# Kernel tuning notes

Hardware: AMD Instinct MI355X
Metric: run time of the kernel (lower is better)

The kernel has to match this reference:

```python
import jax, jax.numpy as jnp
import numpy as np


def _kabsch_rmsd(p, c):
    # p, c: [N, 3]
    pm = jnp.mean(p, axis=0)  # [3]
    cm = jnp.mean(c, axis=0)  # [3]
    # 3x3 cross-covariance
    A = (p - pm).T @ (c - cm)
    U, S, Vt = jnp.linalg.svd(A, full_matrices=False)
    d = jnp.sign(jnp.linalg.det(A))
    # corr_mat = diag([1, 1, d]);  rotation = U @ corr_mat @ Vt
    scale = jnp.concatenate([jnp.ones((2,), dtype=p.dtype), d[None].astype(p.dtype)])
    R = U @ (scale[:, None] * Vt)  # [3,3]
    # translation = pm - R @ cm; aligned coords = (R @ c^T)^T + translation
    aligned = c @ R.T + (pm - R @ cm)
    sq = jnp.sum((p - aligned) ** 2, axis=1)  # [N]
    return jnp.sqrt(jnp.mean(sq))


def setup_inputs() -> dict:
    key = jax.random.key(0)
    k1, k2 = jax.random.split(key)
    B, N = 4096, 2048
    coords_pred = jax.random.normal(k1, (B, N, 3), dtype=jnp.float32)
    coords = jax.random.normal(k2, (B, N, 3), dtype=jnp.float32)
    return {"coords_pred": coords_pred, "coords": coords}


def reference(coords_pred, coords):
    # Batched Kabsch alignment + RMSD; default mode='global', return_all=False
    # -> mean over the per-sample RMSDs.
    rmsds = jax.vmap(_kabsch_rmsd)(coords_pred, coords)  # [B]
    return jnp.mean(rmsds)
```

## Files before the change

kernel.cpp:

```cpp
#include <hip/hip_runtime.h>
#include <math.h>

#define NPTS 2048
#define BLOCK 512
#define NWAVE (BLOCK / 64)

typedef float vfloat4 __attribute__((ext_vector_type(4)));

__global__ __launch_bounds__(BLOCK, 4) void kabsch_kernel(
    const float* __restrict__ P, const float* __restrict__ C,
    float* __restrict__ rmsd_out, int B) {
  const int b = blockIdx.x;
  const int t = threadIdx.x;
  const vfloat4* p4 = (const vfloat4*)(P + (size_t)b * (NPTS * 3));
  const vfloat4* c4 = (const vfloat4*)(C + (size_t)b * (NPTS * 3));

  const int base = 3 * t;
  const vfloat4 pa = __builtin_nontemporal_load(&p4[base]);
  const vfloat4 pb = __builtin_nontemporal_load(&p4[base + 1]);
  const vfloat4 pq = __builtin_nontemporal_load(&p4[base + 2]);
  const vfloat4 ca = __builtin_nontemporal_load(&c4[base]);
  const vfloat4 cb = __builtin_nontemporal_load(&c4[base + 1]);
  const vfloat4 cq = __builtin_nontemporal_load(&c4[base + 2]);

  float acc[17];
#pragma unroll
  for (int i = 0; i < 17; i++) acc[i] = 0.f;

  const float Px[4] = {pa.x, pa.w, pb.z, pq.y};
  const float Py[4] = {pa.y, pb.x, pb.w, pq.z};
  const float Pz[4] = {pa.z, pb.y, pq.x, pq.w};
  const float Cx[4] = {ca.x, ca.w, cb.z, cq.y};
  const float Cy[4] = {ca.y, cb.x, cb.w, cq.z};
  const float Cz[4] = {ca.z, cb.y, cq.x, cq.w};
#pragma unroll
  for (int i = 0; i < 4; i++) {
    const float px = Px[i], py = Py[i], pz = Pz[i];
    const float cx = Cx[i], cy = Cy[i], cz = Cz[i];
    acc[0] += px; acc[1] += py; acc[2] += pz;
    acc[3] += cx; acc[4] += cy; acc[5] += cz;
    acc[6] += px * px + py * py + pz * pz;
    acc[7] += cx * cx + cy * cy + cz * cz;
    acc[8]  += px * cx; acc[9]  += px * cy; acc[10] += px * cz;
    acc[11] += py * cx; acc[12] += py * cy; acc[13] += py * cz;
    acc[14] += pz * cx; acc[15] += pz * cy; acc[16] += pz * cz;
  }

#pragma unroll
  for (int off = 32; off > 0; off >>= 1) {
#pragma unroll
    for (int i = 0; i < 17; i++) acc[i] += __shfl_down(acc[i], off);
  }
  __shared__ float red[NWAVE][17];
  const int wave = t >> 6, lane = t & 63;
  if (lane == 0) {
#pragma unroll
    for (int i = 0; i < 17; i++) red[wave][i] = acc[i];
  }
  __syncthreads();

  if (t == 0) {
    float s[17];
#pragma unroll
    for (int i = 0; i < 17; i++) {
      float v = red[0][i];
#pragma unroll
      for (int w = 1; w < NWAVE; w++) v += red[w][i];
      s[i] = v;
    }
    const float invN = 1.0f / (float)NPTS;
    const float spx = s[0], spy = s[1], spz = s[2];
    const float scx = s[3], scy = s[4], scz = s[5];
    const float Ep = s[6] - (spx * spx + spy * spy + spz * spz) * invN;
    const float Ec = s[7] - (scx * scx + scy * scy + scz * scz) * invN;
    const float a00 = s[8]  - spx * scx * invN, a01 = s[9]  - spx * scy * invN, a02 = s[10] - spx * scz * invN;
    const float a10 = s[11] - spy * scx * invN, a11 = s[12] - spy * scy * invN, a12 = s[13] - spy * scz * invN;
    const float a20 = s[14] - spz * scx * invN, a21 = s[15] - spz * scy * invN, a22 = s[16] - spz * scz * invN;
    const float det = a00 * (a11 * a22 - a12 * a21)
                    - a01 * (a10 * a22 - a12 * a20)
                    + a02 * (a10 * a21 - a11 * a20);
    const float b00 = a00 * a00 + a10 * a10 + a20 * a20;
    const float b11 = a01 * a01 + a11 * a11 + a21 * a21;
    const float b22 = a02 * a02 + a12 * a12 + a22 * a22;
    const float b01 = a00 * a01 + a10 * a11 + a20 * a21;
    const float b02 = a00 * a02 + a10 * a12 + a20 * a22;
    const float b12 = a01 * a02 + a11 * a12 + a21 * a22;
    const float q = (b00 + b11 + b22) * (1.f / 3.f);
    const float p1 = b01 * b01 + b02 * b02 + b12 * b12;
    const float d0 = b00 - q, d1 = b11 - q, d2 = b22 - q;
    const float p2 = d0 * d0 + d1 * d1 + d2 * d2 + 2.f * p1;
    float e1, e2, e3;
    if (p2 < 1e-20f) {
      e1 = e2 = e3 = q;
    } else {
      const float pp = sqrtf(p2 * (1.f / 6.f));
      const float inv = 1.f / pp;
      const float c00 = d0 * inv, c11 = d1 * inv, c22 = d2 * inv;
      const float c01 = b01 * inv, c02 = b02 * inv, c12 = b12 * inv;
      float r = 0.5f * (c00 * (c11 * c22 - c12 * c12)
                      - c01 * (c01 * c22 - c12 * c02)
                      + c02 * (c01 * c12 - c11 * c02));
      r = fminf(1.f, fmaxf(-1.f, r));
      const float phi = acosf(r) * (1.f / 3.f);
      e1 = q + 2.f * pp * cosf(phi);
      e3 = q + 2.f * pp * cosf(phi + 2.0943951023931953f);
      e2 = 3.f * q - e1 - e3;
    }
    const float s1 = sqrtf(fmaxf(e1, 0.f));
    const float s2 = sqrtf(fmaxf(e2, 0.f));
    const float s3 = sqrtf(fmaxf(e3, 0.f));
    const float dsign = (det > 0.f) ? 1.f : ((det < 0.f) ? -1.f : 0.f);
    const float trRS = s1 + s2 + dsign * s3;
    const float msd = (Ep + Ec - 2.f * trRS) * invN;
    rmsd_out[b] = sqrtf(fmaxf(msd, 0.f));
  }
}

__global__ __launch_bounds__(256) void mean_kernel(
    const float* __restrict__ rmsd, float* __restrict__ out, int B) {
  float s = 0.f;
  for (int i = threadIdx.x; i < B; i += 256) s += rmsd[i];
#pragma unroll
  for (int off = 32; off > 0; off >>= 1) s += __shfl_down(s, off);
  __shared__ float sm[4];
  const int wave = threadIdx.x >> 6, lane = threadIdx.x & 63;
  if (lane == 0) sm[wave] = s;
  __syncthreads();
  if (threadIdx.x == 0) {
    float tot = 0.f;
    for (int w = 0; w < 4; w++) tot += sm[w];
    out[0] = tot / (float)B;
  }
}

extern "C" void kernel_launch(void* const* d_in, const int* in_sizes, int n_in,
                              void* d_out, int out_size, void* d_ws, size_t ws_size,
                              hipStream_t stream) {
  const float* P = (const float*)d_in[0];
  const float* C = (const float*)d_in[1];
  float* out = (float*)d_out;
  float* ws = (float*)d_ws;
  const int B = in_sizes[0] / (NPTS * 3);
  kabsch_kernel<<<B, BLOCK, 0, stream>>>(P, C, ws, B);
  mean_kernel<<<1, 256, 0, stream>>>(ws, out, B);
}
```

Measured before the change: 221.5 us.

## Assign one wave per sample with double-buffered register prefetch loop

Each wavefront now processes a whole sample by looping over eight chunks, prefetching the next chunk into registers while accumulating the current one. The block-level shared-memory reduction and __syncthreads are removed, with lane 0 of each wave doing the closed-form SVD/RMSD. This cuts synchronization and block count but gives each thread more serial work and fewer concurrent waves, which may reduce memory-level parallelism.

```diff
diff --git a/kernel.cpp b/kernel.cpp
--- a/kernel.cpp
+++ b/kernel.cpp
@@ -3,47 +3,69 @@
 
 #define NPTS 2048
 #define BLOCK 512
-#define NWAVE (BLOCK / 64)
+#define WPB (BLOCK / 64)
+#define ITERS 8
 
 typedef float vfloat4 __attribute__((ext_vector_type(4)));
 
 __global__ __launch_bounds__(BLOCK, 4) void kabsch_kernel(
     const float* __restrict__ P, const float* __restrict__ C,
     float* __restrict__ rmsd_out, int B) {
-  const int b = blockIdx.x;
-  const int t = threadIdx.x;
+  const int wave = threadIdx.x >> 6;
+  const int lane = threadIdx.x & 63;
+  const int b = blockIdx.x * WPB + wave;
+  if (b >= B) return;
+
   const vfloat4* p4 = (const vfloat4*)(P + (size_t)b * (NPTS * 3));
   const vfloat4* c4 = (const vfloat4*)(C + (size_t)b * (NPTS * 3));
-
-  const int base = 3 * t;
-  const vfloat4 pa = __builtin_nontemporal_load(&p4[base]);
-  const vfloat4 pb = __builtin_nontemporal_load(&p4[base + 1]);
-  const vfloat4 pq = __builtin_nontemporal_load(&p4[base + 2]);
-  const vfloat4 ca = __builtin_nontemporal_load(&c4[base]);
-  const vfloat4 cb = __builtin_nontemporal_load(&c4[base + 1]);
-  const vfloat4 cq = __builtin_nontemporal_load(&c4[base + 2]);
 
   float acc[17];
 #pragma unroll
   for (int i = 0; i < 17; i++) acc[i] = 0.f;
 
-  const float Px[4] = {pa.x, pa.w, pb.z, pq.y};
-  const float Py[4] = {pa.y, pb.x, pb.w, pq.z};
-  const float Pz[4] = {pa.z, pb.y, pq.x, pq.w};
-  const float Cx[4] = {ca.x, ca.w, cb.z, cq.y};
-  const float Cy[4] = {ca.y, cb.x, cb.w, cq.z};
-  const float Cz[4] = {ca.z, cb.y, cq.x, cq.w};
+  vfloat4 bp[2][3], bc[2][3];
+  {
+    const int base = 3 * lane;
+    bp[0][0] = __builtin_nontemporal_load(&p4[base]);
+    bp[0][1] = __builtin_nontemporal_load(&p4[base + 1]);
+    bp[0][2] = __builtin_nontemporal_load(&p4[base + 2]);
+    bc[0][0] = __builtin_nontemporal_load(&c4[base]);
+    bc[0][1] = __builtin_nontemporal_load(&c4[base + 1]);
+    bc[0][2] = __builtin_nontemporal_load(&c4[base + 2]);
+  }
+
 #pragma unroll
-  for (int i = 0; i < 4; i++) {
-    const float px = Px[i], py = Py[i], pz = Pz[i];
-    const float cx = Cx[i], cy = Cy[i], cz = Cz[i];
-    acc[0] += px; acc[1] += py; acc[2] += pz;
-    acc[3] += cx; acc[4] += cy; acc[5] += cz;
-    acc[6] += px * px + py * py + pz * pz;
-    acc[7] += cx * cx + cy * cy + cz * cz;
-    acc[8]  += px * cx; acc[9]  += px * cy; acc[10] += px * cz;
-    acc[11] += py * cx; acc[12] += py * cy; acc[13] += py * cz;
-    acc[14] += pz * cx; acc[15] += pz * cy; acc[16] += pz * cz;
+  for (int k = 0; k < ITERS; k++) {
+    const int cur = k & 1, nxt = cur ^ 1;
+    if (k < ITERS - 1) {
+      const int nb = (k + 1) * 192 + 3 * lane;
+      bp[nxt][0] = __builtin_nontemporal_load(&p4[nb]);
+      bp[nxt][1] = __builtin_nontemporal_load(&p4[nb + 1]);
+      bp[nxt][2] = __builtin_nontemporal_load(&p4[nb + 2]);
+      bc[nxt][0] = __builtin_nontemporal_load(&c4[nb]);
+      bc[nxt][1] = __builtin_nontemporal_load(&c4[nb + 1]);
+      bc[nxt][2] = __builtin_nontemporal_load(&c4[nb + 2]);
+    }
+    const vfloat4 pa = bp[cur][0], pb = bp[cur][1], pq = bp[cur][2];
+    const vfloat4 ca = bc[cur][0], cb = bc[cur][1], cq = bc[cur][2];
+    const float Px[4] = {pa.x, pa.w, pb.z, pq.y};
+    const float Py[4] = {pa.y, pb.x, pb.w, pq.z};
+    const float Pz[4] = {pa.z, pb.y, pq.x, pq.w};
+    const float Cx[4] = {ca.x, ca.w, cb.z, cq.y};
+    const float Cy[4] = {ca.y, cb.x, cb.w, cq.z};
+    const float Cz[4] = {ca.z, cb.y, cq.x, cq.w};
+#pragma unroll
+    for (int i = 0; i < 4; i++) {
+      const float px = Px[i], py = Py[i], pz = Pz[i];
+      const float cx = Cx[i], cy = Cy[i], cz = Cz[i];
+      acc[0] += px; acc[1] += py; acc[2] += pz;
+      acc[3] += cx; acc[4] += cy; acc[5] += cz;
+      acc[6] += px * px + py * py + pz * pz;
+      acc[7] += cx * cx + cy * cy + cz * cz;
+      acc[8]  += px * cx; acc[9]  += px * cy; acc[10] += px * cz;
+      acc[11] += py * cx; acc[12] += py * cy; acc[13] += py * cz;
+      acc[14] += pz * cx; acc[15] += pz * cy; acc[16] += pz * cz;
+    }
   }
 
 #pragma unroll
@@ -51,31 +73,16 @@
 #pragma unroll
     for (int i = 0; i < 17; i++) acc[i] += __shfl_down(acc[i], off);
   }
-  __shared__ float red[NWAVE][17];
-  const int wave = t >> 6, lane = t & 63;
+
   if (lane == 0) {
-#pragma unroll
-    for (int i = 0; i < 17; i++) red[wave][i] = acc[i];
-  }
-  __syncthreads();
-
-  if (t == 0) {
-    float s[17];
-#pragma unroll
-    for (int i = 0; i < 17; i++) {
-      float v = red[0][i];
-#pragma unroll
-      for (int w = 1; w < NWAVE; w++) v += red[w][i];
-      s[i] = v;
-    }
     const float invN = 1.0f / (float)NPTS;
-    const float spx = s[0], spy = s[1], spz = s[2];
-    const float scx = s[3], scy = s[4], scz = s[5];
-    const float Ep = s[6] - (spx * spx + spy * spy + spz * spz) * invN;
-    const float Ec = s[7] - (scx * scx + scy * scy + scz * scz) * invN;
-    const float a00 = s[8]  - spx * scx * invN, a01 = s[9]  - spx * scy * invN, a02 = s[10] - spx * scz * invN;
-    const float a10 = s[11] - spy * scx * invN, a11 = s[12] - spy * scy * invN, a12 = s[13] - spy * scz * invN;
-    const float a20 = s[14] - spz * scx * invN, a21 = s[15] - spz * scy * invN, a22 = s[16] - spz * scz * invN;
+    const float spx = acc[0], spy = acc[1], spz = acc[2];
+    const float scx = acc[3], scy = acc[4], scz = acc[5];
+    const float Ep = acc[6] - (spx * spx + spy * spy + spz * spz) * invN;
+    const float Ec = acc[7] - (scx * scx + scy * scy + scz * scz) * invN;
+    const float a00 = acc[8]  - spx * scx * invN, a01 = acc[9]  - spx * scy * invN, a02 = acc[10] - spx * scz * invN;
+    const float a10 = acc[11] - spy * scx * invN, a11 = acc[12] - spy * scy * invN, a12 = acc[13] - spy * scz * invN;
+    const float a20 = acc[14] - spz * scx * invN, a21 = acc[15] - spz * scy * invN, a22 = acc[16] - spz * scz * invN;
     const float det = a00 * (a11 * a22 - a12 * a21)
                     - a01 * (a10 * a22 - a12 * a20)
                     + a02 * (a10 * a21 - a11 * a20);
@@ -141,6 +148,7 @@
   float* out = (float*)d_out;
   float* ws = (float*)d_ws;
   const int B = in_sizes[0] / (NPTS * 3);
-  kabsch_kernel<<<B, BLOCK, 0, stream>>>(P, C, ws, B);
+  const int grid = (B + WPB - 1) / WPB;
+  kabsch_kernel<<<grid, BLOCK, 0, stream>>>(P, C, ws, B);
   mean_kernel<<<1, 256, 0, stream>>>(ws, out, B);
 }
```

Result: slower. 250.5 us (+13.1%).
